# Kernel optimization log

Hardware: AMD Instinct MI355X
Metric: run time of the kernel (lower is better)

## Reference

```python
import jax, jax.numpy as jnp
from jax import lax
import numpy as np

B = 8; NK = 1024; S = 256; IT_M = 16; IT_R = 16; NC = 5
TH = 0.15; TEMP = 10.0; NREF = 4; BETA = 5.0
MAX_ROT = 45.0; MAX_TRANS = 1.0
BV = B * IT_M          # B_out_v
BIV = BV * IT_R        # B_in_v


def _backproject(cor, d, K):
    # cor [N,S,2] pixels, d [N,S,1] metric depth, K [N,3,3] -> 3D points [N,S,3]
    p = jnp.concatenate([cor, jnp.ones_like(cor[..., :1])], -1)
    Kinv = jnp.linalg.inv(K)
    return d * jnp.einsum('nij,nsj->nsi', Kinv, p)


def _procrustes(X, Y, w):
    # weighted Kabsch: find R,t with Y ~ R X + t.  X,Y [N,S,3], w [N,S]
    sw = w.sum(-1, keepdims=True) + 1e-8
    cx = (w[..., None] * X).sum(1) / sw
    cy = (w[..., None] * Y).sum(1) / sw
    Xc = X - cx[:, None]
    Yc = Y - cy[:, None]
    H = jnp.einsum('ns,nsi,nsj->nij', w, Xc, Yc)
    U, _, Vt = jnp.linalg.svd(H)
    V = jnp.swapaxes(Vt, -1, -2)
    Ut = jnp.swapaxes(U, -1, -2)
    det = jnp.linalg.det(jnp.matmul(V, Ut))
    # R = V diag(1,1,det) U^T  == (V with last column scaled by det) @ U^T
    Vs = jnp.concatenate([V[:, :, :2], V[:, :, 2:] * det[:, None, None]], axis=2)
    R = jnp.matmul(Vs, Ut)
    t = cy - jnp.einsum('nij,nj->ni', R, cx)
    return R, t[:, None, :]


def _resid(X, Y, R, t):
    Yp = jnp.einsum('nij,nsj->nsi', R, X) + t
    return jnp.linalg.norm(Y - Yp, axis=-1)  # [N,S]


def _forward(matches, kps0, kps1, depth0, depth1, T_0to1,
             K_color0, K_color1, Kori_color0, Kori_color1,
             sampled_idx, sampled_idx_ransac):
    f32 = kps0.dtype
    Rgt = T_0to1[:, :3, :3]
    tgt = T_0to1[:, :3, 3]
    # decode flat match index -> (kp0, kp1) indices
    idx0 = sampled_idx // NK
    idx1 = sampled_idx % NK
    bidx = jnp.repeat(jnp.arange(B), IT_M)  # [BV]
    cor0 = jnp.swapaxes(kps0, 1, 2)[bidx[:, None], idx0]   # [BV,S,2]
    cor1 = jnp.swapaxes(kps1, 1, 2)[bidx[:, None], idx1]
    d0 = jnp.swapaxes(depth0, 1, 2)[bidx[:, None], idx0]   # [BV,S,1]
    d1 = jnp.swapaxes(depth1, 1, 2)[bidx[:, None], idx1]
    X = _backproject(cor0, d0, K_color0[bidx])              # [BV,S,3]
    Y = _backproject(cor1, d1, K_color1[bidx])
    # tile over RANSAC hypotheses (matches torch tile(unsqueeze(1)).reshape)
    Xv = jnp.repeat(X, IT_R, axis=0)                        # [BIV,S,3]
    Yv = jnp.repeat(Y, IT_R, axis=0)
    inl0 = jnp.zeros((BIV, S), f32).at[jnp.arange(BIV)[:, None], sampled_idx_ransac].set(1.0)
    # ---- local refinement (no-grad in original) ----
    Xd = lax.stop_gradient(Xv)
    Yd = lax.stop_gradient(Yv)
    inl = inl0
    inl_final = inl0
    pre = jnp.full((BIV,), float(NC), f32)
    for _ in range(NREF):
        Rd, td = _procrustes(Xd, Yd, inl)
        ref = (_resid(Xd, Yd, Rd, td) < TH).astype(f32)
        improved = ref.sum(-1) > pre
        pre = jnp.where(improved, ref.sum(-1), pre)
        inl_final = jnp.where(improved[:, None], inl, inl_final)
        inl = jnp.where(improved[:, None], ref, inl)
    # ---- differentiable final fit + scoring ----
    R, t = _procrustes(Xv, Yv, lax.stop_gradient(inl_final))
    score = jax.nn.sigmoid(BETA * (1.0 - _resid(Xv, Yv, R, t) / TH)).sum(-1)  # soft inlier count [BIV]
    rep = IT_M * IT_R
    Rgt_v = jnp.repeat(Rgt, rep, axis=0)
    tgt_v = jnp.repeat(tgt, rep, axis=0)
    tr = jnp.einsum('nij,nij->n', R, Rgt_v)  # trace(R Rgt^T)
    rot_err = jnp.degrees(jnp.arccos(jnp.clip(0.5 * (tr - 1.0), -1.0 + 1e-6, 1.0 - 1e-6)))
    trans_err = jnp.linalg.norm(t[:, 0, :] - tgt_v, axis=-1)
    # soft-clipped pose losses
    loss_rot_k = (MAX_ROT * jnp.tanh(rot_err / MAX_ROT)).reshape(BV, IT_R)
    loss_trans_k = (MAX_TRANS * jnp.tanh(trans_err / MAX_TRANS)).reshape(BV, IT_R)
    wgt = jax.nn.softmax(score.reshape(BV, IT_R) / TEMP, axis=-1)
    losses_rot = (loss_rot_k * wgt).sum(-1).reshape(B, IT_M).mean(-1, keepdims=True)
    losses_trans = (loss_trans_k * wgt).sum(-1).reshape(B, IT_M).mean(-1, keepdims=True)
    return jnp.stack([losses_rot, losses_trans])  # [2,B,1]


def setup_inputs() -> dict:
    key = jax.random.key(0)
    ks = jax.random.split(key, 10)
    matches = jax.random.uniform(ks[0], (B, NK, NK)) + 1e-6
    kps0 = jax.random.uniform(ks[1], (B, 2, NK)) * 512.0
    kps1 = jax.random.uniform(ks[2], (B, 2, NK)) * 512.0
    depth0 = jax.random.uniform(ks[3], (B, 1, NK)) * 9.5 + 0.5
    depth1 = jax.random.uniform(ks[4], (B, 1, NK)) * 9.5 + 0.5
    Kc = jnp.array([[500.0, 0.0, 256.0], [0.0, 500.0, 256.0], [0.0, 0.0, 1.0]])
    K = jnp.tile(Kc, (B, 1, 1))
    A = jax.random.normal(ks[5], (B, 3, 3))
    Q, _ = jnp.linalg.qr(A)
    Q = Q * jnp.sign(jnp.linalg.det(Q))[:, None, None]  # det = +1
    tv = 0.5 * jax.random.normal(ks[6], (B, 3))
    T = jnp.zeros((B, 4, 4)).at[:, :3, :3].set(Q).at[:, :3, 3].set(tv).at[:, 3, 3].set(1.0)
    sampled_idx = jax.random.randint(ks[7], (BV, S), 0, NK * NK)
    sampled_idx_ransac = jax.random.randint(ks[8], (BIV, NC), 0, S)
    return dict(matches=matches, kps0=kps0, kps1=kps1, depth0=depth0, depth1=depth1,
                T_0to1=T, K_color0=K, K_color1=K, Kori_color0=K, Kori_color1=K,
                sampled_idx=sampled_idx, sampled_idx_ransac=sampled_idx_ransac)


def reference(matches, kps0, kps1, depth0, depth1, T_0to1, K_color0, K_color1,
              Kori_color0, Kori_color1, sampled_idx, sampled_idx_ransac):
    return _forward(matches, kps0, kps1, depth0, depth1, T_0to1, K_color0, K_color1,
                    Kori_color0, Kori_color1, sampled_idx, sampled_idx_ransac)
```

## Files before the change

### kernel.cpp

```cpp
#include <hip/hip_runtime.h>
#include <hip/hip_bf16.h>
#include <math.h>

#ifndef M_PI
#define M_PI 3.14159265358979323846
#endif

namespace mp {

constexpr int NK   = 1024;
constexpr int S    = 256;
constexpr int NREF = 4;
constexpr int BV   = 128;
constexpr int BIV  = 2048;
constexpr int NBLK = BIV / 2;

template <typename T>
__device__ inline T gsum(T v) {
#pragma unroll
  for (int mk = 16; mk >= 1; mk >>= 1) v += __shfl_xor(v, mk, 64);
  return v;
}

__device__ inline void inv3f(const float* __restrict__ K, float Kf[9]) {
  double a = K[0], b = K[1], c = K[2];
  double d = K[3], e = K[4], f = K[5];
  double g = K[6], h = K[7], i = K[8];
  double A  =  (e * i - f * h);
  double Bm = -(d * i - f * g);
  double C  =  (d * h - e * g);
  double det = a * A + b * Bm + c * C;
  double inv = 1.0 / det;
  Kf[0] = (float)(A * inv);  Kf[1] = (float)(-(b * i - c * h) * inv);  Kf[2] = (float)( (b * f - c * e) * inv);
  Kf[3] = (float)(Bm * inv); Kf[4] = (float)( (a * i - c * g) * inv);  Kf[5] = (float)(-(a * f - c * d) * inv);
  Kf[6] = (float)(C * inv);  Kf[7] = (float)(-(a * h - b * g) * inv);  Kf[8] = (float)( (a * e - b * d) * inv);
}

__device__ inline float det3f(float a, float b, float c,
                              float d, float e, float f,
                              float g, float h, float i) {
  return a * (e * i - f * h) - b * (d * i - f * g) + c * (d * h - e * g);
}

__device__ inline void quest_from_acc(const float acc[16], float R[9], float t[3]) {
  float sw = acc[0];
  float rinv = __fdividef(1.0f, sw + 1e-8f);
  float cx[3], cy[3];
#pragma unroll
  for (int i = 0; i < 3; ++i) { cx[i] = acc[1 + i] * rinv; cy[i] = acc[4 + i] * rinv; }
  float H[3][3];
#pragma unroll
  for (int i = 0; i < 3; ++i)
#pragma unroll
    for (int j = 0; j < 3; ++j)
      H[i][j] = acc[7 + 3 * i + j] - cx[i] * acc[4 + j] - acc[1 + i] * cy[j] +
                sw * cx[i] * cy[j];

  float k00 =  H[0][0] + H[1][1] + H[2][2];
  float k11 =  H[0][0] - H[1][1] - H[2][2];
  float k22 = -H[0][0] + H[1][1] - H[2][2];
  float k33 = -H[0][0] - H[1][1] + H[2][2];
  float k01 = H[1][2] - H[2][1];
  float k02 = H[2][0] - H[0][2];
  float k03 = H[0][1] - H[1][0];
  float k12 = H[0][1] + H[1][0];
  float k13 = H[0][2] + H[2][0];
  float k23 = H[1][2] + H[2][1];

  float e2 = (k00 * k11 - k01 * k01) + (k00 * k22 - k02 * k02) +
             (k00 * k33 - k03 * k03) + (k11 * k22 - k12 * k12) +
             (k11 * k33 - k13 * k13) + (k22 * k33 - k23 * k23);
  float e3 = det3f(k00, k01, k02, k01, k11, k12, k02, k12, k22) +
             det3f(k00, k01, k03, k01, k11, k13, k03, k13, k33) +
             det3f(k00, k02, k03, k02, k22, k23, k03, k23, k33) +
             det3f(k11, k12, k13, k12, k22, k23, k13, k23, k33);
  float M00 = det3f(k11, k12, k13, k12, k22, k23, k13, k23, k33);
  float M01 = det3f(k01, k12, k13, k02, k22, k23, k03, k23, k33);
  float M02 = det3f(k01, k11, k13, k02, k12, k23, k03, k13, k33);
  float M03 = det3f(k01, k11, k12, k02, k12, k22, k03, k13, k23);
  float e4 = k00 * M00 - k01 * M01 + k02 * M02 - k03 * M03;

  float g0 = k00 + fabsf(k01) + fabsf(k02) + fabsf(k03);
  float g1 = k11 + fabsf(k01) + fabsf(k12) + fabsf(k13);
  float g2 = k22 + fabsf(k02) + fabsf(k12) + fabsf(k23);
  float g3 = k33 + fabsf(k03) + fabsf(k13) + fabsf(k23);
  float gersh = fmaxf(fmaxf(g0, g1), fmaxf(g2, g3));
  float frob = sqrtf(fmaxf(-2.0f * e2, 0.0f));
  float lam = fmaxf(fminf(gersh, frob), 0.0f) * 1.00001f;

#pragma unroll
  for (int i = 0; i < 9; ++i) {
    float l2 = lam * lam;
    float p  = ((l2 + e2) * lam - e3) * lam + e4;
    float pp = (4.0f * l2 + 2.0f * e2) * lam - e3;
    lam -= __fdividef(p, pp);
  }

  float m00 = k00 - lam, m11 = k11 - lam, m22 = k22 - lam, m33 = k33 - lam;
  float c00 = det3f(m11, k12, k13, k12, m22, k23, k13, k23, m33);
  float c01 = -det3f(k01, k12, k13, k02, m22, k23, k03, k23, m33);
  float c02 = det3f(k01, m11, k13, k02, k12, k23, k03, k13, m33);
  float c03 = -det3f(k01, m11, k12, k02, k12, m22, k03, k13, k23);
  float c11 = det3f(m00, k02, k03, k02, m22, k23, k03, k23, m33);
  float c12 = -det3f(m00, k01, k03, k02, k12, k23, k03, k13, m33);
  float c13 = det3f(m00, k01, k02, k02, k12, m22, k03, k13, k23);
  float c22 = det3f(m00, k01, k03, k01, m11, k13, k03, k13, m33);
  float c23 = -det3f(m00, k01, k02, k01, m11, k12, k03, k13, k23);
  float c33 = det3f(m00, k01, k02, k01, m11, k12, k02, k12, m22);

  float a0 = fabsf(c00), a1 = fabsf(c11), a2 = fabsf(c22), a3 = fabsf(c33);
  float q0 = c00, q1 = c01, q2 = c02, q3 = c03, bb = a0;
  bool t1 = a1 > bb; bb = t1 ? a1 : bb;
  q0 = t1 ? c01 : q0; q1 = t1 ? c11 : q1; q2 = t1 ? c12 : q2; q3 = t1 ? c13 : q3;
  bool t2 = a2 > bb; bb = t2 ? a2 : bb;
  q0 = t2 ? c02 : q0; q1 = t2 ? c12 : q1; q2 = t2 ? c22 : q2; q3 = t2 ? c23 : q3;
  bool t3 = a3 > bb;
  q0 = t3 ? c03 : q0; q1 = t3 ? c13 : q1; q2 = t3 ? c23 : q2; q3 = t3 ? c33 : q3;

  float n2 = q0 * q0 + q1 * q1 + q2 * q2 + q3 * q3;
  bool ok = n2 > 1e-30f;
  float qn = rsqrtf(ok ? n2 : 1.0f);
  float qw = ok ? q0 * qn : 1.0f;
  float qx = ok ? q1 * qn : 0.0f;
  float qy = ok ? q2 * qn : 0.0f;
  float qz = ok ? q3 * qn : 0.0f;

  R[0] = 1.0f - 2.0f * (qy * qy + qz * qz);
  R[1] = 2.0f * (qx * qy - qw * qz);
  R[2] = 2.0f * (qx * qz + qw * qy);
  R[3] = 2.0f * (qx * qy + qw * qz);
  R[4] = 1.0f - 2.0f * (qx * qx + qz * qz);
  R[5] = 2.0f * (qy * qz - qw * qx);
  R[6] = 2.0f * (qx * qz - qw * qy);
  R[7] = 2.0f * (qy * qz + qw * qx);
  R[8] = 1.0f - 2.0f * (qx * qx + qy * qy);
#pragma unroll
  for (int i = 0; i < 3; ++i)
    t[i] = cy[i] - (R[3 * i] * cx[0] + R[3 * i + 1] * cx[1] + R[3 * i + 2] * cx[2]);
}

__device__ inline void fitq_masked(const float X[8][3], const float Y[8][3],
                                   unsigned wm, float R[9], float t[3]) {
  float acc[16];
  acc[0] = (float)__popc(wm);
#pragma unroll
  for (int r = 1; r < 16; ++r) acc[r] = 0.0f;
#pragma unroll
  for (int k = 0; k < 8; ++k) {
    bool w = (wm >> k) & 1u;
    float x0 = w ? X[k][0] : 0.0f, x1 = w ? X[k][1] : 0.0f, x2 = w ? X[k][2] : 0.0f;
    float y0 = Y[k][0], y1 = Y[k][1], y2 = Y[k][2];
    acc[1] += x0; acc[2] += x1; acc[3] += x2;
    acc[4] += w ? y0 : 0.0f; acc[5] += w ? y1 : 0.0f; acc[6] += w ? y2 : 0.0f;
    acc[7]  += x0 * y0; acc[8]  += x0 * y1; acc[9]  += x0 * y2;
    acc[10] += x1 * y0; acc[11] += x1 * y1; acc[12] += x1 * y2;
    acc[13] += x2 * y0; acc[14] += x2 * y1; acc[15] += x2 * y2;
  }
#pragma unroll
  for (int mk = 16; mk >= 1; mk >>= 1)
#pragma unroll
    for (int r = 0; r < 16; ++r) acc[r] += __shfl_xor(acc[r], mk, 64);
  quest_from_acc(acc, R, t);
}

__global__ __launch_bounds__(64) void pose_fit_kernel(
    const float* __restrict__ kps0, const float* __restrict__ kps1,
    const float* __restrict__ depth0, const float* __restrict__ depth1,
    const float* __restrict__ T01,
    const float* __restrict__ K0, const float* __restrict__ K1,
    const int* __restrict__ sidx, const int* __restrict__ sransac,
    float* __restrict__ oscore, float* __restrict__ olr,
    float* __restrict__ olt) {
  const int blk  = blockIdx.x;
  const int lane = threadIdx.x;
  const int grp  = lane >> 5;
  const int gl   = lane & 31;
  const int m = blk * 2 + grp;
  const int v = m >> 4;
  const int b = v >> 4;

  float Kf0[9], Kf1[9];
  inv3f(K0 + b * 9, Kf0);
  inv3f(K1 + b * 9, Kf1);

  int r5[5];
#pragma unroll
  for (int c = 0; c < 5; ++c) r5[c] = sransac[m * 5 + c];
  float w5[5];
#pragma unroll
  for (int c = 0; c < 5; ++c) {
    bool dup = false;
#pragma unroll
    for (int j = 0; j < c; ++j) dup = dup || (r5[j] == r5[c]);
    w5[c] = dup ? 0.0f : 1.0f;
  }

  float accs[16];
#pragma unroll
  for (int r = 0; r < 16; ++r) accs[r] = 0.0f;
#pragma unroll
  for (int c = 0; c < 5; ++c) {
    int idx = sidx[v * S + r5[c]];
    int i0 = idx >> 10;
    int i1 = idx & (NK - 1);
    float u0 = kps0[b * 2 * NK + i0];
    float w0 = kps0[b * 2 * NK + NK + i0];
    float d0 = depth0[b * NK + i0];
    float u1 = kps1[b * 2 * NK + i1];
    float w1 = kps1[b * 2 * NK + NK + i1];
    float d1 = depth1[b * NK + i1];
    float Xc[3], Yc[3];
#pragma unroll
    for (int i = 0; i < 3; ++i) {
      Xc[i] = d0 * (Kf0[3 * i] * u0 + Kf0[3 * i + 1] * w0 + Kf0[3 * i + 2]);
      Yc[i] = d1 * (Kf1[3 * i] * u1 + Kf1[3 * i + 1] * w1 + Kf1[3 * i + 2]);
    }
    float g = w5[c];
    accs[0] += g;
#pragma unroll
    for (int i = 0; i < 3; ++i) {
      float gx = g * Xc[i];
      accs[1 + i] += gx;
      accs[4 + i] += g * Yc[i];
#pragma unroll
      for (int j = 0; j < 3; ++j) accs[7 + 3 * i + j] += gx * Yc[j];
    }
  }

  float X[8][3], Y[8][3];
#pragma unroll
  for (int k = 0; k < 8; ++k) {
    int s = gl + 32 * k;
    int idx = sidx[v * S + s];
    int i0 = idx >> 10;
    int i1 = idx & (NK - 1);
    float u0 = kps0[b * 2 * NK + i0];
    float w0 = kps0[b * 2 * NK + NK + i0];
    float d0 = depth0[b * NK + i0];
    float u1 = kps1[b * 2 * NK + i1];
    float w1 = kps1[b * 2 * NK + NK + i1];
    float d1 = depth1[b * NK + i1];
#pragma unroll
    for (int i = 0; i < 3; ++i) {
      X[k][i] = d0 * (Kf0[3 * i] * u0 + Kf0[3 * i + 1] * w0 + Kf0[3 * i + 2]);
      Y[k][i] = d1 * (Kf1[3 * i] * u1 + Kf1[3 * i + 1] * w1 + Kf1[3 * i + 2]);
    }
  }

  unsigned wm = 0;
#pragma unroll
  for (int c = 0; c < 5; ++c) {
    int r = r5[c];
    if ((r & 31) == gl) wm |= 1u << (r >> 5);
  }

  float R[9], t[3];
  quest_from_acc(accs, R, t);
  unsigned nwm = 0;
  float Rs[9], ts[3], sqs[8];
#pragma unroll
  for (int k = 0; k < 8; ++k) {
    float e0 = Y[k][0] - (R[0] * X[k][0] + R[1] * X[k][1] + R[2] * X[k][2] + t[0]);
    float e1 = Y[k][1] - (R[3] * X[k][0] + R[4] * X[k][1] + R[5] * X[k][2] + t[1]);
    float e2 = Y[k][2] - (R[6] * X[k][0] + R[7] * X[k][1] + R[8] * X[k][2] + t[2]);
    float sq = e0 * e0 + e1 * e1 + e2 * e2;
    sqs[k] = sq;
    nwm |= (sq < 0.0225f) ? (1u << k) : 0u;
  }
#pragma unroll
  for (int i = 0; i < 9; ++i) Rs[i] = R[i];
#pragma unroll
  for (int i = 0; i < 3; ++i) ts[i] = t[i];
  int rs = gsum(__popc(nwm));
  bool imp = rs > 5;
  int pre = imp ? rs : 5;
  wm = imp ? nwm : wm;

  if (__any(imp)) {
    for (int it = 1; it < NREF; ++it) {
      fitq_masked(X, Y, wm, R, t);
      unsigned nw2 = 0;
      float sq32[8];
#pragma unroll
      for (int k = 0; k < 8; ++k) {
        float e0 = Y[k][0] - (R[0] * X[k][0] + R[1] * X[k][1] + R[2] * X[k][2] + t[0]);
        float e1 = Y[k][1] - (R[3] * X[k][0] + R[4] * X[k][1] + R[5] * X[k][2] + t[1]);
        float e2 = Y[k][2] - (R[6] * X[k][0] + R[7] * X[k][1] + R[8] * X[k][2] + t[2]);
        float sq = e0 * e0 + e1 * e1 + e2 * e2;
        sq32[k] = sq;
        nw2 |= (sq < 0.0225f) ? (1u << k) : 0u;
      }
      int rs2 = gsum(__popc(nw2));
      bool imp2 = rs2 > pre;
#pragma unroll
      for (int i = 0; i < 9; ++i) Rs[i] = imp2 ? R[i] : Rs[i];
#pragma unroll
      for (int i = 0; i < 3; ++i) ts[i] = imp2 ? t[i] : ts[i];
#pragma unroll
      for (int k = 0; k < 8; ++k) sqs[k] = imp2 ? sq32[k] : sqs[k];
      pre = imp2 ? rs2 : pre;
      wm  = imp2 ? nw2 : wm;
      if (!__any(imp2)) break;
    }
  }

  float sc = 0.0f;
#pragma unroll
  for (int k = 0; k < 8; ++k) {
    float r = sqrtf(sqs[k]);
    float xar = 5.0f * (1.0f - r * (1.0f / 0.15f));
    sc += 1.0f / (1.0f + __expf(-xar));
  }
  sc = gsum(sc);

  const float* Tb = T01 + b * 16;
  float tr = 0.0f;
#pragma unroll
  for (int i = 0; i < 3; ++i)
#pragma unroll
    for (int j = 0; j < 3; ++j) tr += Rs[i * 3 + j] * Tb[i * 4 + j];
  double xcl = 0.5 * ((double)tr - 1.0);
  const double lo = -1.0 + 1e-6, hi = 1.0 - 1e-6;
  xcl = xcl < lo ? lo : (xcl > hi ? hi : xcl);
  float rot_err = acosf((float)xcl) * (float)(180.0 / M_PI);
  float te0 = ts[0] - Tb[3];
  float te1 = ts[1] - Tb[7];
  float te2 = ts[2] - Tb[11];
  float terr = sqrtf(te0 * te0 + te1 * te1 + te2 * te2);
  float lr = 45.0f * tanhf(rot_err * (1.0f / 45.0f));
  float lt = tanhf(terr);

  if (gl == 0) {
    oscore[m] = sc;
    olr[m] = lr;
    olt[m] = lt;
  }
}

__global__ __launch_bounds__(128) void pose_reduce_kernel(
    const float* __restrict__ oscore, const float* __restrict__ olr,
    const float* __restrict__ olt, float* __restrict__ out) {
  __shared__ float slr[BV], slt[BV];
  int k = threadIdx.x;
  float s[16], mx = -1e30f;
#pragma unroll
  for (int r = 0; r < 16; ++r) {
    s[r] = oscore[k * 16 + r];
    mx = fmaxf(mx, s[r]);
  }
  float den = 0.0f, wl = 0.0f, wt = 0.0f;
#pragma unroll
  for (int r = 0; r < 16; ++r) {
    float e = __expf((s[r] - mx) * 0.1f);
    den += e;
    wl += e * olr[k * 16 + r];
    wt += e * olt[k * 16 + r];
  }
  float di = 1.0f / den;
  slr[k] = wl * di;
  slt[k] = wt * di;
  __syncthreads();
  if (k < 8) {
    float a = 0.0f, c = 0.0f;
#pragma unroll
    for (int i = 0; i < 16; ++i) {
      a += slr[k * 16 + i];
      c += slt[k * 16 + i];
    }
    out[k]     = a * (1.0f / 16.0f);
    out[8 + k] = c * (1.0f / 16.0f);
  }
}

}

extern "C" void kernel_launch(void* const* d_in, const int* in_sizes, int n_in,
                              void* d_out, int out_size, void* d_ws, size_t ws_size,
                              hipStream_t stream) {
  const float* kps0   = (const float*)d_in[1];
  const float* kps1   = (const float*)d_in[2];
  const float* depth0 = (const float*)d_in[3];
  const float* depth1 = (const float*)d_in[4];
  const float* T01    = (const float*)d_in[5];
  const float* K0     = (const float*)d_in[6];
  const float* K1     = (const float*)d_in[7];
  const int* sidx     = (const int*)d_in[10];
  const int* srans    = (const int*)d_in[11];

  float* ws      = (float*)d_ws;
  float* oscore  = ws;
  float* olr     = ws + mp::BIV;
  float* olt     = ws + 2 * mp::BIV;

  mp::pose_fit_kernel<<<mp::NBLK, 64, 0, stream>>>(
      kps0, kps1, depth0, depth1, T01, K0, K1, sidx, srans, oscore, olr, olt);
  mp::pose_reduce_kernel<<<1, 128, 0, stream>>>(
      oscore, olr, olt, (float*)d_out);
}
```

Before: 14.42 us.

## Fuse pose fit and softmax reduction into one kernel with atomic accumulation

Merges the per-hypothesis pose-fit kernel and the single-block reduction kernel into one kernel. Each 512-thread block now handles one outer sample's 16 RANSAC hypotheses, does the softmax-weighted reduction in shared memory and wave shuffles, and atomically adds its share into the output. This removes the second kernel launch and the workspace round trip. In exchange it adds a memset before the launch, float atomics with nondeterministic summation order, and cuts the grid from 1024 small blocks to 128 larger ones.

```diff
diff --git a/kernel.cpp b/kernel.cpp
--- a/kernel.cpp
+++ b/kernel.cpp
@@ -13,7 +13,6 @@
 constexpr int NREF = 4;
 constexpr int BV   = 128;
 constexpr int BIV  = 2048;
-constexpr int NBLK = BIV / 2;
 
 template <typename T>
 __device__ inline T gsum(T v) {
@@ -163,21 +162,23 @@
   quest_from_acc(acc, R, t);
 }
 
-__global__ __launch_bounds__(64) void pose_fit_kernel(
+__global__ __launch_bounds__(512) void pose_kernel(
     const float* __restrict__ kps0, const float* __restrict__ kps1,
     const float* __restrict__ depth0, const float* __restrict__ depth1,
     const float* __restrict__ T01,
     const float* __restrict__ K0, const float* __restrict__ K1,
     const int* __restrict__ sidx, const int* __restrict__ sransac,
-    float* __restrict__ oscore, float* __restrict__ olr,
-    float* __restrict__ olt) {
-  const int blk  = blockIdx.x;
-  const int lane = threadIdx.x;
+    float* __restrict__ out) {
+  const int v    = blockIdx.x;
+  const int wid  = threadIdx.x >> 6;
+  const int lane = threadIdx.x & 63;
   const int grp  = lane >> 5;
   const int gl   = lane & 31;
-  const int m = blk * 2 + grp;
-  const int v = m >> 4;
-  const int b = v >> 4;
+  const int ci   = wid * 2 + grp;
+  const int m    = v * 16 + ci;
+  const int b    = v >> 4;
+
+  __shared__ float sco[16], slr[16], slt[16];
 
   float Kf0[9], Kf1[9];
   inv3f(K0 + b * 9, Kf0);
@@ -331,44 +332,34 @@
   float lt = tanhf(terr);
 
   if (gl == 0) {
-    oscore[m] = sc;
-    olr[m] = lr;
-    olt[m] = lt;
-  }
-}
-
-__global__ __launch_bounds__(128) void pose_reduce_kernel(
-    const float* __restrict__ oscore, const float* __restrict__ olr,
-    const float* __restrict__ olt, float* __restrict__ out) {
-  __shared__ float slr[BV], slt[BV];
-  int k = threadIdx.x;
-  float s[16], mx = -1e30f;
-#pragma unroll
-  for (int r = 0; r < 16; ++r) {
-    s[r] = oscore[k * 16 + r];
-    mx = fmaxf(mx, s[r]);
-  }
-  float den = 0.0f, wl = 0.0f, wt = 0.0f;
-#pragma unroll
-  for (int r = 0; r < 16; ++r) {
-    float e = __expf((s[r] - mx) * 0.1f);
-    den += e;
-    wl += e * olr[k * 16 + r];
-    wt += e * olt[k * 16 + r];
-  }
-  float di = 1.0f / den;
-  slr[k] = wl * di;
-  slt[k] = wt * di;
+    sco[ci] = sc;
+    slr[ci] = lr;
+    slt[ci] = lt;
+  }
   __syncthreads();
-  if (k < 8) {
-    float a = 0.0f, c = 0.0f;
-#pragma unroll
-    for (int i = 0; i < 16; ++i) {
-      a += slr[k * 16 + i];
-      c += slt[k * 16 + i];
-    }
-    out[k]     = a * (1.0f / 16.0f);
-    out[8 + k] = c * (1.0f / 16.0f);
+
+  if (threadIdx.x < 64) {
+    int l = threadIdx.x;
+    bool act = l < 16;
+    float s = act ? sco[l] : -1e30f;
+    float mx = s;
+#pragma unroll
+    for (int mk = 1; mk <= 8; mk <<= 1) mx = fmaxf(mx, __shfl_xor(mx, mk, 64));
+    float e  = act ? __expf((s - mx) * 0.1f) : 0.0f;
+    float wl = act ? e * slr[l] : 0.0f;
+    float wt = act ? e * slt[l] : 0.0f;
+    float den = e;
+#pragma unroll
+    for (int mk = 1; mk <= 8; mk <<= 1) {
+      den += __shfl_xor(den, mk, 64);
+      wl  += __shfl_xor(wl, mk, 64);
+      wt  += __shfl_xor(wt, mk, 64);
+    }
+    if (l == 0) {
+      float di = 1.0f / den;
+      atomicAdd(&out[b],     wl * di * (1.0f / 16.0f));
+      atomicAdd(&out[8 + b], wt * di * (1.0f / 16.0f));
+    }
   }
 }
 
@@ -387,13 +378,7 @@
   const int* sidx     = (const int*)d_in[10];
   const int* srans    = (const int*)d_in[11];
 
-  float* ws      = (float*)d_ws;
-  float* oscore  = ws;
-  float* olr     = ws + mp::BIV;
-  float* olt     = ws + 2 * mp::BIV;
-
-  mp::pose_fit_kernel<<<mp::NBLK, 64, 0, stream>>>(
-      kps0, kps1, depth0, depth1, T01, K0, K1, sidx, srans, oscore, olr, olt);
-  mp::pose_reduce_kernel<<<1, 128, 0, stream>>>(
-      oscore, olr, olt, (float*)d_out);
-}
+  hipMemsetAsync(d_out, 0, 16 * sizeof(float), stream);
+  mp::pose_kernel<<<mp::BV, 512, 0, stream>>>(
+      kps0, kps1, depth0, depth1, T01, K0, K1, sidx, srans, (float*)d_out);
+}
```

After: 22.82 us. 1.58x slower.
